# Optimization experiments

Measured on AMD Instinct MI355X. Metric: run time of the kernel, lower is better.

## Reference

```python
import jax, jax.numpy as jnp
import numpy as np

N = 40000
C_IN, C_OUT = 64, 128
SHAPE = (512, 16, 512)   # (x, height, z); dim=1 -> n_kernels=16
BEV_H, BEV_W = 512, 512  # bev_dims = [0, 2]
N_KERNELS = 16
BATCH = 2


def setup_inputs() -> dict:
    key = jax.random.key(0)
    k1, k2, k3, k4, k5, k6 = jax.random.split(key, 6)
    x = jax.random.randint(k1, (N,), 0, BEV_H, dtype=jnp.int32)
    h = jax.random.randint(k2, (N,), 0, N_KERNELS, dtype=jnp.int32)
    z = jax.random.randint(k3, (N,), 0, BEV_W, dtype=jnp.int32)
    b = jax.random.randint(k4, (N,), 0, BATCH, dtype=jnp.int32)
    coords = jnp.stack([x, h, z, b], axis=1)  # [N, 4]
    feats = jax.random.normal(k5, (N, C_IN), dtype=jnp.float32)
    std = 1.0 / np.sqrt(C_IN)
    kernel = jax.random.uniform(k6, (N_KERNELS, C_IN, C_OUT), dtype=jnp.float32,
                                minval=-std, maxval=std)
    return {"coords": coords, "feats": feats, "kernel": kernel,
            "stride": 1, "batch_size": BATCH}


def reference(coords, feats, kernel, stride, batch_size):
    # gather per-point kernel by height bin (dim=1), offset is zero
    kidx = coords[:, 1] // stride                      # [N]
    per_point_k = kernel[kidx]                         # [N, C_in, C_out]
    f = jnp.einsum('nc,nco->no', feats, per_point_k)   # [N, C_out]
    # flat BEV index: batch * (H*W) + x * W + z
    b = coords[:, 3].astype(jnp.int32)
    xb = (coords[:, 0] // stride).astype(jnp.int32)
    zb = (coords[:, 2] // stride).astype(jnp.int32)
    idx = b * (BEV_H * BEV_W) + xb * BEV_W + zb        # [N]
    num_seg = batch_size * BEV_H * BEV_W
    dense = jax.ops.segment_sum(f, idx, num_segments=num_seg)  # [B*H*W, C_out]
    out = dense.reshape(batch_size, BEV_H, BEV_W, C_OUT)
    return jnp.transpose(out, (0, 3, 1, 2))            # [B, C_out, H, W]
```

## Files before the change

### kernel.cpp

```cpp
#include <hip/hip_runtime.h>


#define CIN    64
#define COUT   128
#define BEVH   512
#define BEVW   512
#define HW     (BEVH * BEVW)
#define NBINS  16
#define PTS_PER_WAVE  8
#define PTS_PER_BLOCK 32

__global__ __launch_bounds__(256) void bev_sort(
    const int* __restrict__ coords,
    const int* __restrict__ stride_p,
    int*       __restrict__ head,
    int*       __restrict__ blkhist,
    int*       __restrict__ sorted,
    int n, int nblk, int scap, int ncells)
{
    __shared__ int hist[NBINS];
    const int tid = threadIdx.x;
    const int vb  = blockIdx.x;

    {
        int4* h4 = (int4*)head;
        const int tot4 = ncells >> 2;
        const int zero_stride = nblk * 256;
        for (int i = vb * 256 + tid; i < tot4; i += zero_stride)
            h4[i] = make_int4(0, 0, 0, 0);
    }

    if (tid < NBINS) hist[tid] = 0;
    __syncthreads();

    const int i = vb * 256 + tid;
    int k = 0, rank = 0;
    if (i < n) {
        k = coords[i * 4 + 1] / stride_p[0];
        rank = atomicAdd(&hist[k], 1);
    }
    __syncthreads();
    if (i < n)
        sorted[k * scap + vb * 256 + rank] = i;
    if (tid < NBINS)
        blkhist[vb * NBINS + tid] = hist[tid];
}

__global__ __launch_bounds__(256) void bev_point(
    const int*   __restrict__ coords,
    const float* __restrict__ feats,
    const float* __restrict__ kern,
    const int*   __restrict__ stride_p,
    const int*   __restrict__ blkhist,
    const int*   __restrict__ sorted,
    float*       __restrict__ f,
    int*         __restrict__ head,
    int*         __restrict__ nxt,
    int n, int nblk, int scap)
{
    __shared__ float lk[CIN * COUT];
    __shared__ int psum[256];
    __shared__ int sc[256];
    __shared__ int tot[NBINS];
    __shared__ int cbase[NBINS + 1];

    const int tid = threadIdx.x;

    {
        const int bin16 = tid & 15;
        const int seg   = tid >> 4;
        const int per   = (nblk + 15) >> 4;
        const int rlo   = seg * per;
        int rhi = rlo + per; if (rhi > nblk) rhi = nblk;
        int s = 0;
        for (int vb = rlo; vb < rhi; ++vb) s += blkhist[vb * NBINS + bin16];
        psum[tid] = s;
    }
    __syncthreads();
    if (tid < NBINS) {
        int s = 0;
#pragma unroll
        for (int g = 0; g < 16; ++g) s += psum[g * 16 + tid];
        tot[tid] = s;
    }
    __syncthreads();
    if (tid == 0) {
        int acc = 0;
        cbase[0] = 0;
        for (int k = 0; k < NBINS; ++k) {
            acc += (tot[k] + PTS_PER_BLOCK - 1) / PTS_PER_BLOCK;
            cbase[k + 1] = acc;
        }
    }
    __syncthreads();

    const int c = blockIdx.x;
    if (c >= cbase[NBINS]) return;

    int bin = 0;
    while (cbase[bin + 1] <= c) ++bin;
    const int chunk = c - cbase[bin];
    const int cnt   = tot[bin];

    {
        int v = (tid < nblk) ? blkhist[tid * NBINS + bin] : 0;
        sc[tid] = v;
        __syncthreads();
        for (int off = 1; off < 256; off <<= 1) {
            const int add = (tid >= off) ? sc[tid - off] : 0;
            __syncthreads();
            sc[tid] += add;
            __syncthreads();
        }
    }

    {
        const float4* src = (const float4*)(kern + (size_t)bin * CIN * COUT);
        float4* dst = (float4*)lk;
#pragma unroll
        for (int j = 0; j < 8; ++j)
            dst[j * 256 + tid] = src[j * 256 + tid];
    }
    __syncthreads();

    const int wave = tid >> 6;
    const int lane = tid & 63;
    const int r0 = chunk * PTS_PER_BLOCK + wave * PTS_PER_WAVE;
    const int navail = cnt - r0;
    if (navail <= 0) return;
    const int np = navail < PTS_PER_WAVE ? navail : PTS_PER_WAVE;

    int pts[PTS_PER_WAVE];
#pragma unroll
    for (int p = 0; p < PTS_PER_WAVE; ++p) {
        const int rr = (p < np) ? (r0 + p) : r0;
        int lo = 0, hi = nblk;
        while (lo < hi) {
            const int mid = (lo + hi) >> 1;
            if (sc[mid] > rr) hi = mid; else lo = mid + 1;
        }
        const int local = rr - (lo ? sc[lo - 1] : 0);
        pts[p] = __builtin_amdgcn_readfirstlane(sorted[bin * scap + lo * 256 + local]);
    }

    float ax[PTS_PER_WAVE], ay[PTS_PER_WAVE];
#pragma unroll
    for (int p = 0; p < PTS_PER_WAVE; ++p) { ax[p] = 0.f; ay[p] = 0.f; }

#pragma unroll
    for (int cc = 0; cc < CIN; ++cc) {
        const float2 kv = *(const float2*)&lk[cc * COUT + 2 * lane];
#pragma unroll
        for (int p = 0; p < PTS_PER_WAVE; ++p) {
            const float fv = feats[(size_t)pts[p] * CIN + cc];
            ax[p] = fmaf(fv, kv.x, ax[p]);
            ay[p] = fmaf(fv, kv.y, ay[p]);
        }
    }

#pragma unroll
    for (int p = 0; p < PTS_PER_WAVE; ++p) {
        if (p < np)
            *(float2*)(f + (size_t)pts[p] * COUT + 2 * lane) = make_float2(ax[p], ay[p]);
    }

    if (lane == 0) {
        const int stride = stride_p[0];
        for (int p = 0; p < np; ++p) {
            const int pt = pts[p];
            const int cx = coords[pt * 4 + 0];
            const int cz = coords[pt * 4 + 2];
            const int cb = coords[pt * 4 + 3];
            const int cell = (cb << 18) + ((cx / stride) << 9) + (cz / stride);
            const int old = atomicExch(&head[cell], pt + 1);
            nxt[pt] = old;
        }
    }
}

__global__ __launch_bounds__(256) void bev_accum(
    const int* __restrict__ coords,
    const int* __restrict__ stride_p,
    float*     __restrict__ f,
    const int* __restrict__ head,
    const int* __restrict__ nxt,
    int n)
{
    const int wave = threadIdx.x >> 6;
    const int lane = threadIdx.x & 63;
    int pt = blockIdx.x * 4 + wave;
    if (pt >= n) return;
    pt = __builtin_amdgcn_readfirstlane(pt);

    const int nx0 = __builtin_amdgcn_readfirstlane(nxt[pt]);
    if (nx0 == 0) return;

    const int stride = stride_p[0];
    const int cx = coords[pt * 4 + 0];
    const int cz = coords[pt * 4 + 2];
    const int cb = coords[pt * 4 + 3];
    const int cell = (cb << 18) + ((cx / stride) << 9) + (cz / stride);
    if (__builtin_amdgcn_readfirstlane(head[cell]) != pt + 1) return;

    float2 acc = *(const float2*)(f + (size_t)pt * COUT + 2 * lane);
    int p = nx0;
    while (p) {
        const float2 v = *(const float2*)(f + (size_t)(p - 1) * COUT + 2 * lane);
        acc.x += v.x; acc.y += v.y;
        p = __builtin_amdgcn_readfirstlane(nxt[p - 1]);
    }
    *(float2*)(f + (size_t)pt * COUT + 2 * lane) = acc;
}

__global__ __launch_bounds__(256) void bev_dense_row(
    const float* __restrict__ f,
    const int*   __restrict__ head,
    float*       __restrict__ out,
    int nrows)
{
    const int wave = threadIdx.x >> 6;
    const int lane = threadIdx.x & 63;
    const int row = blockIdx.x * 4 + wave;
    if (row >= nrows) return;

    const int x = row & 511;
    const int o = (row >> 9) & 127;
    const int b = row >> 16;
    const int* hrow = head + (b << 18) + (x << 9);
    float* const orow = out + (size_t)row * 512;

#pragma unroll
    for (int h = 0; h < 2; ++h) {
        const int z = h * 256 + lane * 4;
        const int4 h4 = *(const int4*)(hrow + z);
        float4 v = make_float4(0.f, 0.f, 0.f, 0.f);
        if (h4.x) v.x = f[(size_t)(h4.x - 1) * COUT + o];
        if (h4.y) v.y = f[(size_t)(h4.y - 1) * COUT + o];
        if (h4.z) v.z = f[(size_t)(h4.z - 1) * COUT + o];
        if (h4.w) v.w = f[(size_t)(h4.w - 1) * COUT + o];
        *(float4*)(orow + z) = v;
    }
}

extern "C" void kernel_launch(void* const* d_in, const int* in_sizes, int n_in,
                              void* d_out, int out_size, void* d_ws, size_t ws_size,
                              hipStream_t stream) {
    const int*   coords   = (const int*)d_in[0];
    const float* feats    = (const float*)d_in[1];
    const float* kern     = (const float*)d_in[2];
    const int*   stride_p = (const int*)d_in[3];
    float* out = (float*)d_out;

    const int n      = in_sizes[0] / 4;
    const int ncells = out_size / COUT;
    const int nblk   = (n + 255) / 256;
    const int scap   = nblk * 256;

    size_t off = 0;
    float* f      = (float*)((char*)d_ws + off); off += (size_t)n * COUT * sizeof(float);
    int* head     = (int*)((char*)d_ws + off);   off += (size_t)ncells * sizeof(int);
    int* nxt      = (int*)((char*)d_ws + off);   off += (size_t)n * sizeof(int);
    int* blkhist  = (int*)((char*)d_ws + off);   off += (size_t)nblk * NBINS * sizeof(int);
    int* sorted   = (int*)((char*)d_ws + off);   off += (size_t)NBINS * scap * sizeof(int);

    bev_sort<<<nblk, 256, 0, stream>>>(coords, stride_p, head, blkhist, sorted,
                                       n, nblk, scap, ncells);

    const int max_chunks = (n + PTS_PER_BLOCK - 1) / PTS_PER_BLOCK + NBINS;
    bev_point<<<max_chunks, 256, 0, stream>>>(coords, feats, kern, stride_p,
                                              blkhist, sorted, f, head, nxt,
                                              n, nblk, scap);

    bev_accum<<<(n + 3) / 4, 256, 0, stream>>>(coords, stride_p, f, head, nxt, n);

    const int nrows = out_size / 512;
    bev_dense_row<<<nrows / 4, 256, 0, stream>>>(f, head, out, nrows);
}
```

Baseline: 357.8 us.

## Reuse head loads across output channels in dense scatter; use wave-shuffle prefix scan

The dense output kernel now has each wave handle 4 output channels per row. It loads the head indices once and fetches a float4 of features per occupied cell instead of one scalar, which cuts redundant head reads and scattered gathers by about 4x. The block-level prefix scan in bev_point is replaced with a wave-level shuffle scan plus a small cross-wave combine, removing many barriers. The dense kernel is dominated by writing the large output, so the gain may be limited by write bandwidth.

```diff
diff --git a/kernel.cpp b/kernel.cpp
--- a/kernel.cpp
+++ b/kernel.cpp
@@ -61,10 +61,13 @@
     __shared__ float lk[CIN * COUT];
     __shared__ int psum[256];
     __shared__ int sc[256];
+    __shared__ int wsum[4];
     __shared__ int tot[NBINS];
     __shared__ int cbase[NBINS + 1];
 
-    const int tid = threadIdx.x;
+    const int tid  = threadIdx.x;
+    const int wave = tid >> 6;
+    const int lane = tid & 63;
 
     {
         const int bin16 = tid & 15;
@@ -104,14 +107,19 @@
 
     {
         int v = (tid < nblk) ? blkhist[tid * NBINS + bin] : 0;
-        sc[tid] = v;
+#pragma unroll
+        for (int off = 1; off < 64; off <<= 1) {
+            const int t = __shfl_up(v, (unsigned)off, 64);
+            if (lane >= off) v += t;
+        }
+        if (lane == 63) wsum[wave] = v;
         __syncthreads();
-        for (int off = 1; off < 256; off <<= 1) {
-            const int add = (tid >= off) ? sc[tid - off] : 0;
-            __syncthreads();
-            sc[tid] += add;
-            __syncthreads();
-        }
+        int add = 0;
+#pragma unroll
+        for (int w = 0; w < 3; ++w)
+            if (w < wave) add += wsum[w];
+        sc[tid] = v + add;
+        __syncthreads();
     }
 
     {
@@ -123,8 +131,6 @@
     }
     __syncthreads();
 
-    const int wave = tid >> 6;
-    const int lane = tid & 63;
     const int r0 = chunk * PTS_PER_BLOCK + wave * PTS_PER_WAVE;
     const int navail = cnt - r0;
     if (navail <= 0) return;
@@ -212,33 +218,36 @@
     *(float2*)(f + (size_t)pt * COUT + 2 * lane) = acc;
 }
 
-__global__ __launch_bounds__(256) void bev_dense_row(
+__global__ __launch_bounds__(256) void bev_dense_o16(
     const float* __restrict__ f,
     const int*   __restrict__ head,
-    float*       __restrict__ out,
-    int nrows)
-{
+    float*       __restrict__ out)
+{
+    const int bid  = blockIdx.x;
     const int wave = threadIdx.x >> 6;
     const int lane = threadIdx.x & 63;
-    const int row = blockIdx.x * 4 + wave;
-    if (row >= nrows) return;
-
-    const int x = row & 511;
-    const int o = (row >> 9) & 127;
-    const int b = row >> 16;
+    const int og = bid & 7;
+    const int x  = (bid >> 3) & 511;
+    const int b  = bid >> 12;
+    const int o0 = og * 16 + wave * 4;
+
     const int* hrow = head + (b << 18) + (x << 9);
-    float* const orow = out + (size_t)row * 512;
+    float* const obase = out + (((size_t)(b * COUT + o0)) << 18) + ((size_t)x << 9);
 
 #pragma unroll
     for (int h = 0; h < 2; ++h) {
         const int z = h * 256 + lane * 4;
         const int4 h4 = *(const int4*)(hrow + z);
-        float4 v = make_float4(0.f, 0.f, 0.f, 0.f);
-        if (h4.x) v.x = f[(size_t)(h4.x - 1) * COUT + o];
-        if (h4.y) v.y = f[(size_t)(h4.y - 1) * COUT + o];
-        if (h4.z) v.z = f[(size_t)(h4.z - 1) * COUT + o];
-        if (h4.w) v.w = f[(size_t)(h4.w - 1) * COUT + o];
-        *(float4*)(orow + z) = v;
+        float4 c0 = make_float4(0.f, 0.f, 0.f, 0.f);
+        float4 c1 = c0, c2 = c0, c3 = c0;
+        if (h4.x) c0 = *(const float4*)(f + (size_t)(h4.x - 1) * COUT + o0);
+        if (h4.y) c1 = *(const float4*)(f + (size_t)(h4.y - 1) * COUT + o0);
+        if (h4.z) c2 = *(const float4*)(f + (size_t)(h4.z - 1) * COUT + o0);
+        if (h4.w) c3 = *(const float4*)(f + (size_t)(h4.w - 1) * COUT + o0);
+        *(float4*)(obase + ((size_t)0 << 18) + z) = make_float4(c0.x, c1.x, c2.x, c3.x);
+        *(float4*)(obase + ((size_t)1 << 18) + z) = make_float4(c0.y, c1.y, c2.y, c3.y);
+        *(float4*)(obase + ((size_t)2 << 18) + z) = make_float4(c0.z, c1.z, c2.z, c3.z);
+        *(float4*)(obase + ((size_t)3 << 18) + z) = make_float4(c0.w, c1.w, c2.w, c3.w);
     }
 }
 
@@ -253,6 +262,7 @@
 
     const int n      = in_sizes[0] / 4;
     const int ncells = out_size / COUT;
+    const int batch  = out_size / (COUT * HW);
     const int nblk   = (n + 255) / 256;
     const int scap   = nblk * 256;
 
@@ -273,6 +283,6 @@
 
     bev_accum<<<(n + 3) / 4, 256, 0, stream>>>(coords, stride_p, f, head, nxt, n);
 
-    const int nrows = out_size / 512;
-    bev_dense_row<<<nrows / 4, 256, 0, stream>>>(f, head, out, nrows);
-}
+    const int ndblocks = batch * BEVH * 8;
+    bev_dense_o16<<<ndblocks, 256, 0, stream>>>(f, head, out);
+}
```

New measurement: 365.1 us. 1.02x slower.
